# Kernel optimization log

Hardware: AMD Instinct MI355X
Metric: run time of the kernel (lower is better)

## Reference

```python
import jax, jax.numpy as jnp
import numpy as np
import math

B, S, E = 4, 2048, 1024
H, KV = 16, 4            # query heads, kv heads
HD = E // H              # head_dim = 64
R, CD = 8, 64            # TPA rank, context dim
NQ, NL = 8, 2            # qubits, VQC layers
EPS = 1e-6
LN_EPS = 1e-5


def setup_inputs() -> dict:
    key = jax.random.key(0)
    ks = jax.random.split(key, 16)
    def dense(k, i, o):
        return (jax.random.normal(k, (i, o), jnp.float32) / np.float32(np.sqrt(i)))
    d = {}
    d["x"] = jax.random.normal(ks[0], (B, S, E), jnp.float32)
    d["ctxW"] = dense(ks[1], E, CD);      d["ctxb"] = jnp.zeros((CD,), jnp.float32)
    d["qaW"] = dense(ks[2], E, R * HD);   d["qab"] = jnp.zeros((R * HD,), jnp.float32)
    d["qbW"] = dense(ks[3], CD, R * H);   d["qbb"] = jnp.zeros((R * H,), jnp.float32)
    d["kaW"] = dense(ks[4], E, R * HD);   d["kab"] = jnp.zeros((R * HD,), jnp.float32)
    d["kbW"] = dense(ks[5], CD, R * KV);  d["kbb"] = jnp.zeros((R * KV,), jnp.float32)
    d["vaW"] = dense(ks[6], E, R * HD);   d["vab"] = jnp.zeros((R * HD,), jnp.float32)
    d["vbW"] = dense(ks[7], CD, R * KV);  d["vbb"] = jnp.zeros((R * KV,), jnp.float32)
    d["qeW"] = dense(ks[8], HD, NQ);      d["qeb"] = jnp.zeros((NQ,), jnp.float32)
    d["vqc"] = jax.random.normal(ks[9], (NL, NQ, 3), jnp.float32) * 0.3
    d["ent"] = jnp.array([0.1], jnp.float32)
    d["outW"] = dense(ks[10], E, E);      d["outb"] = jnp.zeros((E,), jnp.float32)
    d["gamma"] = jnp.ones((E,), jnp.float32)
    d["beta"] = jnp.zeros((E,), jnp.float32)
    return d


def _tpa(x, ctx, aW, ab, bW, bb, nh):
    # output = sum_r (x @ A_r) outer (ctx @ B_r)  ->  [b, nh, s, head_dim]
    b, s, _ = x.shape
    a = (x @ aW + ab).reshape(b, s, R, HD)
    bf = (ctx @ bW + bb).reshape(b, s, R, nh)
    return jnp.einsum('bsrd,bsrh->bhsd', a, bf)


def _quantum_features(x, qeW, qeb, vqc, ent):
    # x: [b, h, s, HD] -> features [b, h, s, 2*NQ]
    angles = jnp.tanh(x @ qeW + qeb) * math.pi
    f = angles
    for l in range(NL):
        p = vqc[l]  # [NQ, 3]
        f = jnp.cos(f + p[:, 0]) * jnp.sin(f + p[:, 1]) + jnp.cos(f + p[:, 2])
        f = f * (1.0 + ent[0] * jnp.roll(f, shift=1, axis=-1))  # entanglement
    qf = jnp.concatenate([jnp.cos(f), jnp.sin(f)], axis=-1)
    return qf / (jnp.linalg.norm(qf, axis=-1, keepdims=True) + EPS)


def reference(x, ctxW, ctxb, qaW, qab, qbW, qbb, kaW, kab, kbW, kbb,
              vaW, vab, vbW, vbb, qeW, qeb, vqc, ent, outW, outb, gamma, beta):
    ctx = x @ ctxW + ctxb                              # [B,S,CD]
    q = _tpa(x, ctx, qaW, qab, qbW, qbb, H)            # [B,H,S,HD]
    k = _tpa(x, ctx, kaW, kab, kbW, kbb, KV)           # [B,KV,S,HD]
    v = _tpa(x, ctx, vaW, vab, vbW, vbb, KV)
    # GQA: expand KV heads to match query heads
    k = jnp.repeat(k, H // KV, axis=1)
    v = jnp.repeat(v, H // KV, axis=1)
    qf = _quantum_features(q, qeW, qeb, vqc, ent)      # [B,H,S,2*NQ]
    kf = _quantum_features(k, qeW, qeb, vqc, ent)
    # causal linear attention via cumulative KV state
    kv = jnp.cumsum(jnp.einsum('bhsf,bhsd->bhsfd', kf, v), axis=2)
    num = jnp.einsum('bhsf,bhsfd->bhsd', qf, kv)
    den = jnp.einsum('bhsf,bhsf->bhs', qf, jnp.cumsum(kf, axis=2))
    attn = num / (den[..., None] + EPS)                # [B,H,S,HD]
    o = attn.transpose(0, 2, 1, 3).reshape(B, S, E) @ outW + outb
    y = x + o                                          # residual + layernorm
    mu = jnp.mean(y, axis=-1, keepdims=True)
    var = jnp.mean(jnp.square(y - mu), axis=-1, keepdims=True)
    return gamma * (y - mu) / jnp.sqrt(var + LN_EPS) + beta
```

## Files before the change

### kernel.cpp

```cpp
#include <hip/hip_runtime.h>
#include <math.h>

#define Bb  4
#define Ss  2048
#define Ee  1024
#define Hh  16
#define KVh 4
#define HD  64
#define RNK 8
#define CDd 64
#define NQ  8
#define NLn 2
#define NF  16
#define NC  32
#define CT  (Ss/NC)
#define BS  (Bb*Ss)
#define NCAT 1664

typedef unsigned short ushort_t;
typedef __attribute__((ext_vector_type(8))) short short8;
typedef __attribute__((ext_vector_type(4))) float f32x4;

__device__ __forceinline__ unsigned short f2bf(float f) {
    unsigned int u = __float_as_uint(f);
    unsigned int r = (u + 0x7FFFu + ((u >> 16) & 1u)) >> 16;
    return (unsigned short)r;
}
__device__ __forceinline__ float bf2f(unsigned short h) {
    return __uint_as_float(((unsigned int)h) << 16);
}

#define GLD16(gp, lp) \
    __builtin_amdgcn_global_load_lds((const __attribute__((address_space(1))) void*)(gp), \
                                     (__attribute__((address_space(3))) void*)(lp), 16, 0, 0)

__global__ __launch_bounds__(256)
void cast_f32_bf16(const float* __restrict__ in, ushort_t* __restrict__ outp, long n)
{
    long i = ((long)blockIdx.x * blockDim.x + threadIdx.x) * 8;
    if (i >= n) return;
    short8 o;
    #pragma unroll
    for (int j = 0; j < 8; ++j) o[j] = (short)f2bf(in[i + j]);
    *(short8*)(outp + i) = o;
}

__global__ __launch_bounds__(256)
void transpose_cast(const float* __restrict__ W, ushort_t* __restrict__ Wt,
                    int K, int Nsub, int nOff, int ldT)
{
    __shared__ float t[32][33];
    const int k0 = blockIdx.x * 32, n0 = blockIdx.y * 32;
    const int tx = threadIdx.x & 31, ty = threadIdx.x >> 5;
    #pragma unroll
    for (int i = 0; i < 4; ++i)
        t[ty + 8*i][tx] = W[(size_t)(k0 + ty + 8*i) * Nsub + (n0 + tx)];
    __syncthreads();
    #pragma unroll
    for (int i = 0; i < 4; ++i)
        Wt[(size_t)(nOff + n0 + ty + 8*i) * ldT + (k0 + tx)] = f2bf(t[tx][ty + 8*i]);
}

__global__ __launch_bounds__(256)
void transpose_cast3(const float* __restrict__ W0, const float* __restrict__ W1,
                     const float* __restrict__ W2, ushort_t* __restrict__ Wt, int ldT)
{
    __shared__ float t[32][33];
    const int z = blockIdx.z;
    const float* W = (z == 0) ? W0 : (z == 1) ? W1 : W2;
    const int nOff = 512 * z;
    const int k0 = blockIdx.x * 32, n0 = blockIdx.y * 32;
    const int tx = threadIdx.x & 31, ty = threadIdx.x >> 5;
    #pragma unroll
    for (int i = 0; i < 4; ++i)
        t[ty + 8*i][tx] = W[(size_t)(k0 + ty + 8*i) * 512 + (n0 + tx)];
    __syncthreads();
    #pragma unroll
    for (int i = 0; i < 4; ++i)
        Wt[(size_t)(nOff + n0 + ty + 8*i) * ldT + (k0 + tx)] = f2bf(t[tx][ty + 8*i]);
}

__global__ __launch_bounds__(256)
void prep_small(const float* __restrict__ ctxW,
                const float* __restrict__ qab, const float* __restrict__ kab,
                const float* __restrict__ vab, const float* __restrict__ ctxb,
                ushort_t* __restrict__ WcatT, float* __restrict__ bcat)
{
    __shared__ float t[32][33];
    const int bid = blockIdx.x;
    if (bid < 64) {
        const int k0 = (bid >> 1) * 32, n0 = (bid & 1) * 32;
        const int tx = threadIdx.x & 31, ty = threadIdx.x >> 5;
        #pragma unroll
        for (int i = 0; i < 4; ++i)
            t[ty + 8*i][tx] = ctxW[(size_t)(k0 + ty + 8*i) * 64 + (n0 + tx)];
        __syncthreads();
        #pragma unroll
        for (int i = 0; i < 4; ++i)
            WcatT[(size_t)(1536 + n0 + ty + 8*i) * Ee + (k0 + tx)] = f2bf(t[tx][ty + 8*i]);
    } else if (bid < 96) {
        const int idx = (bid - 64) * 2048 + threadIdx.x * 8;
        short8 z = {0, 0, 0, 0, 0, 0, 0, 0};
        *(short8*)(WcatT + (size_t)1600 * Ee + idx) = z;
    } else {
        const int n = (bid - 96) * 256 + threadIdx.x;
        if (n < NCAT) {
            float v = 0.f;
            if      (n < 512)  v = qab[n];
            else if (n < 1024) v = kab[n - 512];
            else if (n < 1536) v = vab[n - 1024];
            else if (n < 1600) v = ctxb[n - 1536];
            bcat[n] = v;
        }
    }
}

template<int RES, int OUTBF>
__global__ __launch_bounds__(256)
void gemm_mfma(const ushort_t* __restrict__ A, const ushort_t* __restrict__ Bt,
               const float* __restrict__ bias, const float* __restrict__ res,
               void* __restrict__ Cout, int M, int N, int K)
{
    __shared__ ushort_t Al[128 * 32];
    __shared__ ushort_t Bl[128 * 32];
    const int tid  = threadIdx.x;
    const int lane = tid & 63;
    const int wave = tid >> 6;
    const int wm = wave >> 1;
    const int wn = wave & 1;

    const unsigned nx  = gridDim.x;
    const unsigned bid = blockIdx.y * nx + blockIdx.x;
    const unsigned nwg = nx * gridDim.y;
    const unsigned qc = nwg >> 3, rc = nwg & 7;
    const unsigned xc = bid & 7, of = bid >> 3;
    const unsigned tile = (xc < rc ? xc * (qc + 1) : rc * (qc + 1) + (xc - rc) * qc) + of;
    const int bm = (int)(tile / nx) * 128;
    const int bn = (int)(tile % nx) * 128;

    f32x4 acc[4][4] = {};

    const int arow0 = wave * 16 + (lane >> 2);
    const int kq = lane & 3;
    const ushort_t* Ag0 = A  + (size_t)(bm + arow0) * K + kq * 8;
    const ushort_t* Ag1 = A  + (size_t)(bm + 64 + arow0) * K + kq * 8;
    const ushort_t* Bg0 = Bt + (size_t)(bn + arow0) * K + kq * 8;
    const ushort_t* Bg1 = Bt + (size_t)(bn + 64 + arow0) * K + kq * 8;
    ushort_t* Alw = Al + wave * 512;
    ushort_t* Blw = Bl + wave * 512;

    const int fr = lane & 15;
    const int fg = lane >> 4;

    for (int k0 = 0; k0 < K; k0 += 32) {
        GLD16(Ag0 + k0, Alw);
        GLD16(Ag1 + k0, Alw + 2048);
        GLD16(Bg0 + k0, Blw);
        GLD16(Bg1 + k0, Blw + 2048);
        __syncthreads();
        short8 af[4], bfv[4];
        #pragma unroll
        for (int mi = 0; mi < 4; ++mi)
            af[mi] = *(const short8*)&Al[(wm*64 + mi*16 + fr) * 32 + fg * 8];
        #pragma unroll
        for (int ni = 0; ni < 4; ++ni)
            bfv[ni] = *(const short8*)&Bl[(wn*64 + ni*16 + fr) * 32 + fg * 8];
        #pragma unroll
        for (int mi = 0; mi < 4; ++mi)
            #pragma unroll
            for (int ni = 0; ni < 4; ++ni)
                acc[mi][ni] = __builtin_amdgcn_mfma_f32_16x16x32_bf16(
                    af[mi], bfv[ni], acc[mi][ni], 0, 0, 0);
        __syncthreads();
    }

    float bv[4];
    #pragma unroll
    for (int ni = 0; ni < 4; ++ni) bv[ni] = bias[bn + wn*64 + ni*16 + fr];
    #pragma unroll
    for (int mi = 0; mi < 4; ++mi) {
        #pragma unroll
        for (int ni = 0; ni < 4; ++ni) {
            const int gn = bn + wn*64 + ni*16 + fr;
            #pragma unroll
            for (int r = 0; r < 4; ++r) {
                const int gm = bm + wm*64 + mi*16 + fg*4 + r;
                float v = acc[mi][ni][r] + bv[ni];
                if (RES) v += res[(size_t)gm * N + gn];
                if (OUTBF) ((ushort_t*)Cout)[(size_t)gm * N + gn] = f2bf(v);
                else       ((float*)Cout)[(size_t)gm * N + gn] = v;
            }
        }
    }
}

__global__ __launch_bounds__(256)
void combine_quantum(const ushort_t* __restrict__ Cf,
                     const float* __restrict__ qbW, const float* __restrict__ qbb,
                     const float* __restrict__ kbW, const float* __restrict__ kbb,
                     const float* __restrict__ vbW, const float* __restrict__ vbb,
                     const float* __restrict__ qeW, const float* __restrict__ qeb,
                     const float* __restrict__ vqc, const float* __restrict__ ent,
                     float* __restrict__ qf_g, float* __restrict__ kf_g,
                     float* __restrict__ v_g)
{
    const int wid = threadIdx.x >> 6;
    const int d   = threadIdx.x & 63;
    const int bs  = blockIdx.x * 4 + wid;
    const int b = bs >> 11;
    const int s = bs & 2047;

    __shared__ float qew_s[HD*NQ];
    __shared__ float ctx_l[4][CDd];
    __shared__ float bfq[4][128];
    __shared__ float bfk[4][32];
    __shared__ float bfv[4][32];
    __shared__ float rows[4][Hh+KVh][65];

    #pragma unroll
    for (int i = 0; i < 2; ++i)
        qew_s[threadIdx.x + 256*i] = qeW[threadIdx.x + 256*i];

    const ushort_t* Crow = Cf + (size_t)bs * NCAT;
    ctx_l[wid][d] = bf2f(Crow[1536 + d]);
    __syncthreads();

    {
        float q0 = qbb[d], q1 = qbb[d + 64];
        float kv = (d < 32) ? kbb[d] : vbb[d - 32];
        const float* Wkv = (d < 32) ? (kbW + d) : (vbW + (d - 32));
        #pragma unroll 8
        for (int k = 0; k < CDd; ++k) {
            const float c = ctx_l[wid][k];
            q0 += c * qbW[(size_t)k*128 + d];
            q1 += c * qbW[(size_t)k*128 + d + 64];
            kv += c * Wkv[(size_t)k*32];
        }
        bfq[wid][d] = q0; bfq[wid][d + 64] = q1;
        if (d < 32) bfk[wid][d] = kv; else bfv[wid][d - 32] = kv;
    }

    float aq[RNK], ak[RNK], av[RNK];
    #pragma unroll
    for (int r = 0; r < RNK; ++r) {
        aq[r] = bf2f(Crow[r*64 + d]);
        ak[r] = bf2f(Crow[512 + r*64 + d]);
        av[r] = bf2f(Crow[1024 + r*64 + d]);
    }
    __syncthreads();

    #pragma unroll
    for (int h = 0; h < Hh; ++h) {
        float acc = 0.f;
        #pragma unroll
        for (int r = 0; r < RNK; ++r) acc += aq[r] * bfq[wid][r*16 + h];
        rows[wid][h][d] = acc;
    }
    #pragma unroll
    for (int kvh = 0; kvh < KVh; ++kvh) {
        float acck = 0.f, accv = 0.f;
        #pragma unroll
        for (int r = 0; r < RNK; ++r) {
            acck += ak[r] * bfk[wid][r*4 + kvh];
            accv += av[r] * bfv[wid][r*4 + kvh];
        }
        rows[wid][Hh + kvh][d] = acck;
        v_g[((size_t)(b*KVh + kvh)*Ss + s)*HD + d] = accv;
    }
    __syncthreads();

    const float entv = ent[0];
    const int i   = d & 7;
    const int src = (d & ~7) | ((i + 7) & 7);
    float p00 = vqc[(0*NQ + i)*3 + 0], p01 = vqc[(0*NQ + i)*3 + 1], p02 = vqc[(0*NQ + i)*3 + 2];
    float p10 = vqc[(1*NQ + i)*3 + 0], p11 = vqc[(1*NQ + i)*3 + 1], p12 = vqc[(1*NQ + i)*3 + 2];
    const float qebi = qeb[i];

    #pragma unroll
    for (int stripe = 0; stripe < 3; ++stripe) {
        const int row = stripe * 8 + (d >> 3);
        const bool active = (row < Hh + KVh);
        const int rowc = active ? row : (Hh + KVh - 1);
        float acc = qebi;
        #pragma unroll 16
        for (int dd = 0; dd < HD; ++dd)
            acc += rows[wid][rowc][dd] * qew_s[dd*8 + i];
        float f = tanhf(acc) * 3.14159265358979323846f;
        float g = cosf(f + p00) * sinf(f + p01) + cosf(f + p02);
        float gp = __shfl(g, src, 64);
        f = g * (1.f + entv * gp);
        g = cosf(f + p10) * sinf(f + p11) + cosf(f + p12);
        gp = __shfl(g, src, 64);
        f = g * (1.f + entv * gp);
        float c = cosf(f), sn = sinf(f);
        float ss = c*c + sn*sn;
        ss += __shfl_xor(ss, 1, 64);
        ss += __shfl_xor(ss, 2, 64);
        ss += __shfl_xor(ss, 4, 64);
        const float inv = 1.f / (sqrtf(ss) + 1e-6f);
        if (active) {
            float* dst = (row < Hh)
                ? qf_g + ((size_t)(b*Hh + row)*Ss + s)*NF
                : kf_g + ((size_t)(b*KVh + (row - Hh))*Ss + s)*NF;
            dst[i]      = c * inv;
            dst[NQ + i] = sn * inv;
        }
    }
}

__global__ __launch_bounds__(64)
void chunk_partial(const float* __restrict__ kf_g, const float* __restrict__ v_g,
                   float* __restrict__ kvpart, float* __restrict__ kfpart)
{
    const int id = blockIdx.x;
    const int c = id & (NC-1);
    const int bk = id / NC;
    const int d = threadIdx.x;
    __shared__ float kf_l[CT][NF];
    const int s0 = c * CT;
    const float* kfp = kf_g + ((size_t)bk*Ss + s0)*NF;
    #pragma unroll
    for (int t = 0; t < (CT*NF)/64; ++t)
        ((float*)kf_l)[d + 64*t] = kfp[d + 64*t];
    __syncthreads();
    float st[NF] = {};
    const float* vp = v_g + ((size_t)bk*Ss + s0)*HD;
    for (int t = 0; t < CT; ++t) {
        const float vd = vp[(size_t)t*HD + d];
        #pragma unroll
        for (int f = 0; f < NF; ++f) st[f] += kf_l[t][f] * vd;
    }
    float* kvp = kvpart + (size_t)id * (NF*HD);
    #pragma unroll
    for (int f = 0; f < NF; ++f) kvp[f*HD + d] = st[f];
    if (d < NF) {
        float acc = 0.f;
        for (int t = 0; t < CT; ++t) acc += kf_l[t][d];
        kfpart[(size_t)id*NF + d] = acc;
    }
}

__global__ void prefix_scan(float* __restrict__ kvpart, float* __restrict__ kfpart)
{
    const int idx = blockIdx.x * blockDim.x + threadIdx.x;
    const int total = Bb*KVh * (NF*HD + NF);
    if (idx >= total) return;
    const int bk = idx / (NF*HD + NF);
    const int e = idx % (NF*HD + NF);
    if (e < NF*HD) {
        float* p = kvpart + (size_t)bk*NC*(NF*HD) + e;
        float run = 0.f;
        for (int c = 0; c < NC; ++c) {
            const float t = p[(size_t)c*(NF*HD)];
            p[(size_t)c*(NF*HD)] = run;
            run += t;
        }
    } else {
        const int f = e - NF*HD;
        float* p = kfpart + (size_t)bk*NC*NF + f;
        float run = 0.f;
        for (int c = 0; c < NC; ++c) {
            const float t = p[(size_t)c*NF];
            p[(size_t)c*NF] = run;
            run += t;
        }
    }
}

__global__ __launch_bounds__(64)
void attn_scan(const float* __restrict__ qf_g, const float* __restrict__ kf_g,
               const float* __restrict__ v_g,
               const float* __restrict__ kvpart, const float* __restrict__ kfpart,
               ushort_t* __restrict__ o_bf)
{
    const int id = blockIdx.x;
    const int c = id & (NC-1);
    const int bh = id / NC;
    const int h = bh & (Hh-1);
    const int b = bh / Hh;
    const int kvh = h >> 2;
    const int d = threadIdx.x;
    __shared__ float kf_l[CT][NF];
    __shared__ float qf_l[CT][NF];
    const int s0 = c * CT;
    const float* kfp = kf_g + ((size_t)(b*KVh + kvh)*Ss + s0)*NF;
    const float* qfp = qf_g + ((size_t)(b*Hh + h)*Ss + s0)*NF;
    #pragma unroll
    for (int t = 0; t < (CT*NF)/64; ++t) {
        ((float*)kf_l)[d + 64*t] = kfp[d + 64*t];
        ((float*)qf_l)[d + 64*t] = qfp[d + 64*t];
    }
    float st[NF], kfs[NF];
    const float* kvp = kvpart + ((size_t)(b*KVh + kvh)*NC + c)*(NF*HD);
    const float* kfsp = kfpart + ((size_t)(b*KVh + kvh)*NC + c)*NF;
    #pragma unroll
    for (int f = 0; f < NF; ++f) { st[f] = kvp[f*HD + d]; kfs[f] = kfsp[f]; }
    __syncthreads();
    const float* vp = v_g + ((size_t)(b*KVh + kvh)*Ss + s0)*HD;
    ushort_t* op = o_bf + ((size_t)(b*Ss + s0))*Ee + h*HD;
    for (int t = 0; t < CT; ++t) {
        const float vd = vp[(size_t)t*HD + d];
        float num0 = 0.f, num1 = 0.f, den0 = 0.f, den1 = 0.f;
        #pragma unroll
        for (int f = 0; f < NF; f += 2) {
            const float kv0 = kf_l[t][f];
            const float kv1 = kf_l[t][f+1];
            st[f]   += kv0 * vd;   kfs[f]   += kv0;
            st[f+1] += kv1 * vd;   kfs[f+1] += kv1;
            const float qv0 = qf_l[t][f];
            const float qv1 = qf_l[t][f+1];
            num0 += qv0 * st[f];   den0 += qv0 * kfs[f];
            num1 += qv1 * st[f+1]; den1 += qv1 * kfs[f+1];
        }
        op[(size_t)t*Ee + d] = f2bf((num0 + num1) / ((den0 + den1) + 1e-6f));
    }
}

__global__ __launch_bounds__(256)
void layernorm_res(const float* __restrict__ x, const ushort_t* __restrict__ o_bf,
                   const float* __restrict__ gamma, const float* __restrict__ beta,
                   float* __restrict__ out)
{
    __shared__ float tmp[4];
    const int row = blockIdx.x;
    const int t = threadIdx.x;
    const float* xp = x + (size_t)row * Ee;
    const ushort_t* op = o_bf + (size_t)row * Ee;
    float v[4];
    float sum = 0.f;
    #pragma unroll
    for (int i = 0; i < 4; ++i) {
        const int n = t + 256*i;
        v[i] = xp[n] + bf2f(op[n]);
        sum += v[i];
    }
    #pragma unroll
    for (int o = 32; o > 0; o >>= 1) sum += __shfl_down(sum, o, 64);
    if ((t & 63) == 0) tmp[t >> 6] = sum;
    __syncthreads();
    const float mu = (tmp[0] + tmp[1] + tmp[2] + tmp[3]) * (1.f/Ee);
    __syncthreads();
    float vs = 0.f;
    #pragma unroll
    for (int i = 0; i < 4; ++i) { const float dd = v[i] - mu; vs += dd*dd; }
    #pragma unroll
    for (int o = 32; o > 0; o >>= 1) vs += __shfl_down(vs, o, 64);
    if ((t & 63) == 0) tmp[t >> 6] = vs;
    __syncthreads();
    const float var = (tmp[0] + tmp[1] + tmp[2] + tmp[3]) * (1.f/Ee);
    const float inv = rsqrtf(var + 1e-5f);
    float* pout = out + (size_t)row * Ee;
    #pragma unroll
    for (int i = 0; i < 4; ++i) {
        const int n = t + 256*i;
        pout[n] = gamma[n] * (v[i] - mu) * inv + beta[n];
    }
}

extern "C" void kernel_launch(void* const* d_in, const int* in_sizes, int n_in,
                              void* d_out, int out_size, void* d_ws, size_t ws_size,
                              hipStream_t stream)
{
    const float* x    = (const float*)d_in[0];
    const float* ctxW = (const float*)d_in[1];
    const float* ctxb = (const float*)d_in[2];
    const float* qaW  = (const float*)d_in[3];
    const float* qab  = (const float*)d_in[4];
    const float* qbW  = (const float*)d_in[5];
    const float* qbb  = (const float*)d_in[6];
    const float* kaW  = (const float*)d_in[7];
    const float* kab  = (const float*)d_in[8];
    const float* kbW  = (const float*)d_in[9];
    const float* kbb  = (const float*)d_in[10];
    const float* vaW  = (const float*)d_in[11];
    const float* vab  = (const float*)d_in[12];
    const float* vbW  = (const float*)d_in[13];
    const float* vbb  = (const float*)d_in[14];
    const float* qeW  = (const float*)d_in[15];
    const float* qeb  = (const float*)d_in[16];
    const float* vqc  = (const float*)d_in[17];
    const float* ent  = (const float*)d_in[18];
    const float* outW = (const float*)d_in[19];
    const float* outb = (const float*)d_in[20];
    const float* gamma= (const float*)d_in[21];
    const float* beta = (const float*)d_in[22];
    float* out = (float*)d_out;

    char* p = (char*)d_ws;
    auto alloc = [&](size_t bytes) { char* r = p; p += (bytes + 255) & ~(size_t)255; return (void*)r; };
    ushort_t* xb    = (ushort_t*)alloc((size_t)BS * Ee * 2);
    ushort_t* WcatT = (ushort_t*)alloc((size_t)NCAT * Ee * 2);
    ushort_t* outWt = (ushort_t*)alloc((size_t)Ee * Ee * 2);
    float*    bcat  = (float*)   alloc(NCAT * 4);
    ushort_t* Cf    = (ushort_t*)alloc((size_t)BS * NCAT * 2);
    float*    qf    = (float*)   alloc((size_t)Bb*Hh*Ss*NF * 4);
    float*    kf    = (float*)   alloc((size_t)Bb*KVh*Ss*NF * 4);
    float*    vg    = (float*)   alloc((size_t)Bb*KVh*Ss*HD * 4);
    float*    kvpart= (float*)   alloc((size_t)Bb*KVh*NC*NF*HD * 4);
    float*    kfpart= (float*)   alloc((size_t)Bb*KVh*NC*NF * 4);
    ushort_t* obf2  = (ushort_t*)alloc((size_t)BS * Ee * 2);
    ushort_t* obf   = Cf;

    cast_f32_bf16<<<(BS*(long)Ee/8 + 255)/256, 256, 0, stream>>>(x, xb, (long)BS*Ee);
    transpose_cast3<<<dim3(32, 16, 3), 256, 0, stream>>>(qaW, kaW, vaW, WcatT, Ee);
    prep_small<<<103, 256, 0, stream>>>(ctxW, qab, kab, vab, ctxb, WcatT, bcat);
    transpose_cast<<<dim3(32, 32), 256, 0, stream>>>(outW, outWt, Ee, 1024, 0, Ee);

    gemm_mfma<0,1><<<dim3(NCAT/128, BS/128), 256, 0, stream>>>(
        xb, WcatT, bcat, nullptr, Cf, BS, NCAT, Ee);
    combine_quantum<<<BS/4, 256, 0, stream>>>(Cf, qbW, qbb, kbW, kbb, vbW, vbb,
                                              qeW, qeb, vqc, ent, qf, kf, vg);
    chunk_partial<<<Bb*KVh*NC, 64, 0, stream>>>(kf, vg, kvpart, kfpart);
    prefix_scan<<<(Bb*KVh*(NF*HD + NF) + 255)/256, 256, 0, stream>>>(kvpart, kfpart);
    attn_scan<<<Bb*Hh*NC, 64, 0, stream>>>(qf, kf, vg, kvpart, kfpart, obf);
    gemm_mfma<0,1><<<dim3(Ee/128, BS/128), 256, 0, stream>>>(
        obf, outWt, outb, nullptr, obf2, BS, Ee, Ee);
    layernorm_res<<<BS, 256, 0, stream>>>(x, obf2, gamma, beta, out);
}
```

Before: 301.9 us.

## Merge weight prep launches, drop prefix scan kernel, vectorize layernorm

Folds the three weight transpose/cast kernels into one launch, which cuts launch overhead. It removes the separate prefix_scan kernel: each attn_scan block now sums the earlier chunk partials itself. That adds redundant reads that grow with chunk index, up to 31 chunks of 1 KB. The layernorm loads and stores become 4-wide vectors, and the second GEMM output buffer reuses the qf workspace instead of a new allocation.

```diff
diff --git a/kernel.cpp b/kernel.cpp
--- a/kernel.cpp
+++ b/kernel.cpp
@@ -20,6 +20,7 @@
 typedef unsigned short ushort_t;
 typedef __attribute__((ext_vector_type(8))) short short8;
 typedef __attribute__((ext_vector_type(4))) float f32x4;
+typedef __attribute__((ext_vector_type(4))) unsigned short u16x4;
 
 __device__ __forceinline__ unsigned short f2bf(float f) {
     unsigned int u = __float_as_uint(f);
@@ -46,71 +47,65 @@
 }
 
 __global__ __launch_bounds__(256)
-void transpose_cast(const float* __restrict__ W, ushort_t* __restrict__ Wt,
-                    int K, int Nsub, int nOff, int ldT)
-{
-    __shared__ float t[32][33];
-    const int k0 = blockIdx.x * 32, n0 = blockIdx.y * 32;
-    const int tx = threadIdx.x & 31, ty = threadIdx.x >> 5;
-    #pragma unroll
-    for (int i = 0; i < 4; ++i)
-        t[ty + 8*i][tx] = W[(size_t)(k0 + ty + 8*i) * Nsub + (n0 + tx)];
-    __syncthreads();
-    #pragma unroll
-    for (int i = 0; i < 4; ++i)
-        Wt[(size_t)(nOff + n0 + ty + 8*i) * ldT + (k0 + tx)] = f2bf(t[tx][ty + 8*i]);
-}
-
-__global__ __launch_bounds__(256)
-void transpose_cast3(const float* __restrict__ W0, const float* __restrict__ W1,
-                     const float* __restrict__ W2, ushort_t* __restrict__ Wt, int ldT)
-{
-    __shared__ float t[32][33];
-    const int z = blockIdx.z;
-    const float* W = (z == 0) ? W0 : (z == 1) ? W1 : W2;
-    const int nOff = 512 * z;
-    const int k0 = blockIdx.x * 32, n0 = blockIdx.y * 32;
-    const int tx = threadIdx.x & 31, ty = threadIdx.x >> 5;
-    #pragma unroll
-    for (int i = 0; i < 4; ++i)
-        t[ty + 8*i][tx] = W[(size_t)(k0 + ty + 8*i) * 512 + (n0 + tx)];
-    __syncthreads();
-    #pragma unroll
-    for (int i = 0; i < 4; ++i)
-        Wt[(size_t)(nOff + n0 + ty + 8*i) * ldT + (k0 + tx)] = f2bf(t[tx][ty + 8*i]);
-}
-
-__global__ __launch_bounds__(256)
-void prep_small(const float* __restrict__ ctxW,
-                const float* __restrict__ qab, const float* __restrict__ kab,
-                const float* __restrict__ vab, const float* __restrict__ ctxb,
-                ushort_t* __restrict__ WcatT, float* __restrict__ bcat)
+void weight_prep(const float* __restrict__ qaW, const float* __restrict__ kaW,
+                 const float* __restrict__ vaW, const float* __restrict__ outW,
+                 const float* __restrict__ ctxW,
+                 const float* __restrict__ qab, const float* __restrict__ kab,
+                 const float* __restrict__ vab, const float* __restrict__ ctxb,
+                 ushort_t* __restrict__ WcatT, ushort_t* __restrict__ outWt,
+                 float* __restrict__ bcat)
 {
     __shared__ float t[32][33];
     const int bid = blockIdx.x;
-    if (bid < 64) {
-        const int k0 = (bid >> 1) * 32, n0 = (bid & 1) * 32;
-        const int tx = threadIdx.x & 31, ty = threadIdx.x >> 5;
+    const int tx = threadIdx.x & 31, ty = threadIdx.x >> 5;
+    if (bid < 1536) {
+        const int z = bid >> 9;
+        const int r = bid & 511;
+        const int k0 = (r & 31) * 32, n0 = (r >> 5) * 32;
+        const float* W = (z == 0) ? qaW : (z == 1) ? kaW : vaW;
+        const int nOff = 512 * z;
         #pragma unroll
         for (int i = 0; i < 4; ++i)
-            t[ty + 8*i][tx] = ctxW[(size_t)(k0 + ty + 8*i) * 64 + (n0 + tx)];
+            t[ty + 8*i][tx] = W[(size_t)(k0 + ty + 8*i) * 512 + (n0 + tx)];
         __syncthreads();
         #pragma unroll
         for (int i = 0; i < 4; ++i)
-            WcatT[(size_t)(1536 + n0 + ty + 8*i) * Ee + (k0 + tx)] = f2bf(t[tx][ty + 8*i]);
-    } else if (bid < 96) {
-        const int idx = (bid - 64) * 2048 + threadIdx.x * 8;
-        short8 z = {0, 0, 0, 0, 0, 0, 0, 0};
-        *(short8*)(WcatT + (size_t)1600 * Ee + idx) = z;
+            WcatT[(size_t)(nOff + n0 + ty + 8*i) * Ee + (k0 + tx)] = f2bf(t[tx][ty + 8*i]);
+    } else if (bid < 2560) {
+        const int r = bid - 1536;
+        const int k0 = (r & 31) * 32, n0 = (r >> 5) * 32;
+        #pragma unroll
+        for (int i = 0; i < 4; ++i)
+            t[ty + 8*i][tx] = outW[(size_t)(k0 + ty + 8*i) * 1024 + (n0 + tx)];
+        __syncthreads();
+        #pragma unroll
+        for (int i = 0; i < 4; ++i)
+            outWt[(size_t)(n0 + ty + 8*i) * Ee + (k0 + tx)] = f2bf(t[tx][ty + 8*i]);
     } else {
-        const int n = (bid - 96) * 256 + threadIdx.x;
-        if (n < NCAT) {
-            float v = 0.f;
-            if      (n < 512)  v = qab[n];
-            else if (n < 1024) v = kab[n - 512];
-            else if (n < 1536) v = vab[n - 1024];
-            else if (n < 1600) v = ctxb[n - 1536];
-            bcat[n] = v;
+        const int pid = bid - 2560;
+        if (pid < 64) {
+            const int k0 = (pid >> 1) * 32, n0 = (pid & 1) * 32;
+            #pragma unroll
+            for (int i = 0; i < 4; ++i)
+                t[ty + 8*i][tx] = ctxW[(size_t)(k0 + ty + 8*i) * 64 + (n0 + tx)];
+            __syncthreads();
+            #pragma unroll
+            for (int i = 0; i < 4; ++i)
+                WcatT[(size_t)(1536 + n0 + ty + 8*i) * Ee + (k0 + tx)] = f2bf(t[tx][ty + 8*i]);
+        } else if (pid < 96) {
+            const int idx = (pid - 64) * 2048 + threadIdx.x * 8;
+            short8 z = {0, 0, 0, 0, 0, 0, 0, 0};
+            *(short8*)(WcatT + (size_t)1600 * Ee + idx) = z;
+        } else {
+            const int n = (pid - 96) * 256 + threadIdx.x;
+            if (n < NCAT) {
+                float v = 0.f;
+                if      (n < 512)  v = qab[n];
+                else if (n < 1024) v = kab[n - 512];
+                else if (n < 1536) v = vab[n - 1024];
+                else if (n < 1600) v = ctxb[n - 1536];
+                bcat[n] = v;
+            }
         }
     }
 }
@@ -340,33 +335,6 @@
     }
 }
 
-__global__ void prefix_scan(float* __restrict__ kvpart, float* __restrict__ kfpart)
-{
-    const int idx = blockIdx.x * blockDim.x + threadIdx.x;
-    const int total = Bb*KVh * (NF*HD + NF);
-    if (idx >= total) return;
-    const int bk = idx / (NF*HD + NF);
-    const int e = idx % (NF*HD + NF);
-    if (e < NF*HD) {
-        float* p = kvpart + (size_t)bk*NC*(NF*HD) + e;
-        float run = 0.f;
-        for (int c = 0; c < NC; ++c) {
-            const float t = p[(size_t)c*(NF*HD)];
-            p[(size_t)c*(NF*HD)] = run;
-            run += t;
-        }
-    } else {
-        const int f = e - NF*HD;
-        float* p = kfpart + (size_t)bk*NC*NF + f;
-        float run = 0.f;
-        for (int c = 0; c < NC; ++c) {
-            const float t = p[(size_t)c*NF];
-            p[(size_t)c*NF] = run;
-            run += t;
-        }
-    }
-}
-
 __global__ __launch_bounds__(64)
 void attn_scan(const float* __restrict__ qf_g, const float* __restrict__ kf_g,
                const float* __restrict__ v_g,
@@ -390,11 +358,18 @@
         ((float*)kf_l)[d + 64*t] = kfp[d + 64*t];
         ((float*)qf_l)[d + 64*t] = qfp[d + 64*t];
     }
-    float st[NF], kfs[NF];
-    const float* kvp = kvpart + ((size_t)(b*KVh + kvh)*NC + c)*(NF*HD);
-    const float* kfsp = kfpart + ((size_t)(b*KVh + kvh)*NC + c)*NF;
-    #pragma unroll
-    for (int f = 0; f < NF; ++f) { st[f] = kvp[f*HD + d]; kfs[f] = kfsp[f]; }
+    float st[NF] = {};
+    float kfs[NF] = {};
+    const int bk = b*KVh + kvh;
+    for (int cc = 0; cc < c; ++cc) {
+        const float* kvp = kvpart + ((size_t)bk*NC + cc)*(NF*HD);
+        const float* kfq = kfpart + ((size_t)bk*NC + cc)*NF;
+        #pragma unroll
+        for (int f = 0; f < NF; ++f) {
+            st[f]  += kvp[f*HD + d];
+            kfs[f] += kfq[f];
+        }
+    }
     __syncthreads();
     const float* vp = v_g + ((size_t)(b*KVh + kvh)*Ss + s0)*HD;
     ushort_t* op = o_bf + ((size_t)(b*Ss + s0))*Ee + h*HD;
@@ -426,14 +401,12 @@
     const int t = threadIdx.x;
     const float* xp = x + (size_t)row * Ee;
     const ushort_t* op = o_bf + (size_t)row * Ee;
+    const f32x4 xv = *(const f32x4*)(xp + t*4);
+    const u16x4 ov = *(const u16x4*)(op + t*4);
     float v[4];
     float sum = 0.f;
     #pragma unroll
-    for (int i = 0; i < 4; ++i) {
-        const int n = t + 256*i;
-        v[i] = xp[n] + bf2f(op[n]);
-        sum += v[i];
-    }
+    for (int i = 0; i < 4; ++i) { v[i] = xv[i] + bf2f(ov[i]); sum += v[i]; }
     #pragma unroll
     for (int o = 32; o > 0; o >>= 1) sum += __shfl_down(sum, o, 64);
     if ((t & 63) == 0) tmp[t >> 6] = sum;
@@ -449,12 +422,12 @@
     __syncthreads();
     const float var = (tmp[0] + tmp[1] + tmp[2] + tmp[3]) * (1.f/Ee);
     const float inv = rsqrtf(var + 1e-5f);
-    float* pout = out + (size_t)row * Ee;
-    #pragma unroll
-    for (int i = 0; i < 4; ++i) {
-        const int n = t + 256*i;
-        pout[n] = gamma[n] * (v[i] - mu) * inv + beta[n];
-    }
+    const f32x4 gv = *(const f32x4*)(gamma + t*4);
+    const f32x4 bv = *(const f32x4*)(beta + t*4);
+    f32x4 ovec;
+    #pragma unroll
+    for (int i = 0; i < 4; ++i) ovec[i] = gv[i] * (v[i] - mu) * inv + bv[i];
+    *(f32x4*)(out + (size_t)row * Ee + t*4) = ovec;
 }
 
 extern "C" void kernel_launch(void* const* d_in, const int* in_sizes, int n_in,
@@ -498,20 +471,18 @@
     float*    vg    = (float*)   alloc((size_t)Bb*KVh*Ss*HD * 4);
     float*    kvpart= (float*)   alloc((size_t)Bb*KVh*NC*NF*HD * 4);
     float*    kfpart= (float*)   alloc((size_t)Bb*KVh*NC*NF * 4);
-    ushort_t* obf2  = (ushort_t*)alloc((size_t)BS * Ee * 2);
     ushort_t* obf   = Cf;
+    ushort_t* obf2  = (ushort_t*)qf;
 
     cast_f32_bf16<<<(BS*(long)Ee/8 + 255)/256, 256, 0, stream>>>(x, xb, (long)BS*Ee);
-    transpose_cast3<<<dim3(32, 16, 3), 256, 0, stream>>>(qaW, kaW, vaW, WcatT, Ee);
-    prep_small<<<103, 256, 0, stream>>>(ctxW, qab, kab, vab, ctxb, WcatT, bcat);
-    transpose_cast<<<dim3(32, 32), 256, 0, stream>>>(outW, outWt, Ee, 1024, 0, Ee);
+    weight_prep<<<2663, 256, 0, stream>>>(qaW, kaW, vaW, outW, ctxW,
+                                          qab, kab, vab, ctxb, WcatT, outWt, bcat);
 
     gemm_mfma<0,1><<<dim3(NCAT/128, BS/128), 256, 0, stream>>>(
         xb, WcatT, bcat, nullptr, Cf, BS, NCAT, Ee);
     combine_quantum<<<BS/4, 256, 0, stream>>>(Cf, qbW, qbb, kbW, kbb, vbW, vbb,
                                               qeW, qeb, vqc, ent, qf, kf, vg);
     chunk_partial<<<Bb*KVh*NC, 64, 0, stream>>>(kf, vg, kvpart, kfpart);
-    prefix_scan<<<(Bb*KVh*(NF*HD + NF) + 255)/256, 256, 0, stream>>>(kvpart, kfpart);
     attn_scan<<<Bb*Hh*NC, 64, 0, stream>>>(qf, kf, vg, kvpart, kfpart, obf);
     gemm_mfma<0,1><<<dim3(Ee/128, BS/128), 256, 0, stream>>>(
         obf, outWt, outb, nullptr, obf2, BS, Ee, Ee);
```

New measurement: 303.6 us. About the same (+0.5%).
